# Performance work log

Measured on AMD Instinct MI355X. Metric: run time of the kernel, lower is better.

## Reference

```python
import jax, jax.numpy as jnp
import numpy as np

NUM_EMBEDDINGS = 1024
EMBEDDING_DIM = 256
COMMITMENT_COST = 0.25
DECAY = 0.99
EPSILON = 1e-05


def setup_inputs() -> dict:
    key = jax.random.key(0)
    k1, k2, k3 = jax.random.split(key, 3)
    z = jax.random.normal(k1, (32, EMBEDDING_DIM, 32, 32), dtype=jnp.float32)
    codebook = jax.random.normal(k2, (NUM_EMBEDDINGS, EMBEDDING_DIM), dtype=jnp.float32)
    ema_cluster_size = jnp.zeros((NUM_EMBEDDINGS,), dtype=jnp.float32)
    ema_dw = jax.random.normal(k3, (NUM_EMBEDDINGS, EMBEDDING_DIM), dtype=jnp.float32)
    return {"z": z, "codebook": codebook, "ema_cluster_size": ema_cluster_size, "ema_dw": ema_dw}


def reference(z, codebook, ema_cluster_size, ema_dw):
    K, D = codebook.shape
    # (B,C,H,W) -> (B,H,W,C)
    zp = jnp.transpose(z, (0, 2, 3, 1))
    z_flat = zp.reshape(-1, D)  # [N, D]
    N = z_flat.shape[0]

    # squared L2 distances to each code: [N, K]
    distances = (jnp.sum(z_flat ** 2, axis=1, keepdims=True)
                 + jnp.sum(codebook ** 2, axis=1)
                 - 2.0 * z_flat @ codebook.T)
    idx = jnp.argmin(distances, axis=1)  # [N]

    quantized = codebook[idx].reshape(zp.shape)  # [B,H,W,C]

    # training-mode EMA codebook update (one-hot scatter expressed as segment sums)
    counts = jax.ops.segment_sum(jnp.ones((N,), z_flat.dtype), idx, num_segments=K)  # encodings.sum(0)
    dw = jax.ops.segment_sum(z_flat, idx, num_segments=K)                            # encodings.T @ z_flat
    new_cluster_size = ema_cluster_size * DECAY + (1.0 - DECAY) * counts
    new_ema_dw = ema_dw * DECAY + (1.0 - DECAY) * dw
    n = jnp.sum(new_cluster_size)
    cluster_size = (new_cluster_size + EPSILON) / (n + K * EPSILON) * n
    new_codebook = new_ema_dw / cluster_size[:, None]

    commitment_loss = jnp.mean((zp - jax.lax.stop_gradient(quantized)) ** 2)
    loss = COMMITMENT_COST * commitment_loss

    # straight-through estimator
    quantized_st = zp + jax.lax.stop_gradient(quantized - zp)

    avg_probs = counts / N
    perplexity = jnp.exp(-jnp.sum(avg_probs * jnp.log(avg_probs + 1e-10)))

    quantized_out = jnp.transpose(quantized_st, (0, 3, 1, 2))  # back to (B,C,H,W)
    return (quantized_out, loss, perplexity, new_codebook, new_cluster_size, new_ema_dw)
```

## Files before the change

### kernel.cpp

```cpp
#include <hip/hip_runtime.h>
#include <cfloat>
#include <cstdint>

#define B_BATCH 32
#define D_DIM   256
#define HW      1024
#define N_POS   32768
#define K_CODES 1024
#define DECAY_F   0.99f
#define ONE_M_DECAY 0.01f
#define EPS_F   1e-5f

#define OUT_Q    0
#define OUT_LOSS 8388608
#define OUT_PERP 8388609
#define OUT_CB   8388610
#define OUT_NCS  8650754
#define OUT_EDW  8651778


#define WS_COUNTS  0
#define WS_ZNORM   4096
#define WS_BSUM    4100
#define WS_MEMSET  4104
#define WS_CBNORM  4352
#define WS_OFFS    8448
#define WS_CURSOR  12544
#define WS_IDX     16640
#define WS_SORTED  147712
#define WS_CBHI    278784
#define WS_CBLO    803072
#define WS_PART    1327360
#define WS_SCODE   3424512
#define WS_TOTAL   3555584

typedef short s16x8 __attribute__((ext_vector_type(8)));
typedef float f32x4 __attribute__((ext_vector_type(4)));
typedef unsigned long long u64;

__device__ __forceinline__ ushort f2bf_rne(float x) {
    uint u = __float_as_uint(x);
    uint r = (u + 0x7FFF + ((u >> 16) & 1)) >> 16;
    return (ushort)r;
}
__device__ __forceinline__ float bf2f(ushort h) {
    return __uint_as_float(((uint)h) << 16);
}

__device__ __forceinline__ void gload16(const void* g, void* l) {
    __builtin_amdgcn_global_load_lds(
        (const __attribute__((address_space(1))) unsigned*)(uintptr_t)g,
        (__attribute__((address_space(3))) unsigned*)(uintptr_t)l, 16, 0, 0);
}

__global__ __launch_bounds__(256) void prep_ztrans(const float* __restrict__ z,
                                                   const float* __restrict__ cb,
                                                   ushort* __restrict__ zhi,
                                                   ushort* __restrict__ zlo,
                                                   ushort* __restrict__ cbhi,
                                                   ushort* __restrict__ cblo,
                                                   float* __restrict__ cbnorm,
                                                   float* __restrict__ znorm_acc) {
    __shared__ float Zs[2][32][68];
    __shared__ float red[256];
    const int tid = threadIdx.x;

    if (blockIdx.x >= 512) {
        int wave = tid >> 6;
        int lane = tid & 63;
        int k = (blockIdx.x - 512) * 4 + wave;
        float4 v = *(const float4*)&cb[(size_t)k * D_DIM + lane * 4];
        ushort4 h, l;
        h.x = f2bf_rne(v.x); l.x = f2bf_rne(v.x - bf2f(h.x));
        h.y = f2bf_rne(v.y); l.y = f2bf_rne(v.y - bf2f(h.y));
        h.z = f2bf_rne(v.z); l.z = f2bf_rne(v.z - bf2f(h.z));
        h.w = f2bf_rne(v.w); l.w = f2bf_rne(v.w - bf2f(h.w));
        *(ushort4*)&cbhi[(size_t)k * D_DIM + lane * 4] = h;
        *(ushort4*)&cblo[(size_t)k * D_DIM + lane * 4] = l;
        float s = v.x * v.x + v.y * v.y + v.z * v.z + v.w * v.w;
        #pragma unroll
        for (int off = 32; off >= 1; off >>= 1) s += __shfl_xor(s, off);
        if (lane == 0) cbnorm[k] = s;
        return;
    }

    const int n0  = blockIdx.x * 64;
    const int b   = n0 >> 10;
    const int hw0 = n0 & 1023;
    const float* zb = z + (size_t)b * (D_DIM * HW) + hw0;

    const int zd  = tid >> 4;
    const int zcg = tid & 15;
    const int ga  = zcg ^ (((zd >> 3) & 3) << 1);
    const int gb  = zcg ^ ((((zd + 16) >> 3) & 3) << 1);
    const int n   = tid >> 2;
    const int dq  = tid & 3;
    const int zcol = (((n >> 2) ^ (dq << 1)) << 2) | (n & 3);
    float zsum = 0.f;

    {
        float4 va = *(const float4*)&zb[(size_t)zd * HW + zcg * 4];
        float4 vb = *(const float4*)&zb[(size_t)(zd + 16) * HW + zcg * 4];
        *(float4*)&Zs[0][zd][ga * 4] = va;
        *(float4*)&Zs[0][zd + 16][gb * 4] = vb;
    }

    for (int it = 0; it < 8; ++it) {
        const int d0 = it * 32;
        __syncthreads();
        float4 na, nb;
        if (it < 7) {
            na = *(const float4*)&zb[(size_t)(d0 + 32 + zd) * HW + zcg * 4];
            nb = *(const float4*)&zb[(size_t)(d0 + 48 + zd) * HW + zcg * 4];
        }
        {
            s16x8 hv, lv;
            #pragma unroll
            for (int j = 0; j < 8; ++j) {
                float f = Zs[it & 1][dq * 8 + j][zcol];
                zsum += f * f;
                ushort hb = f2bf_rne(f);
                ushort lb = f2bf_rne(f - bf2f(hb));
                hv[j] = (short)hb;
                lv[j] = (short)lb;
            }
            *(s16x8*)&zhi[(size_t)(n0 + n) * D_DIM + d0 + dq * 8] = hv;
            *(s16x8*)&zlo[(size_t)(n0 + n) * D_DIM + d0 + dq * 8] = lv;
        }
        if (it < 7) {
            *(float4*)&Zs[(it + 1) & 1][zd][ga * 4] = na;
            *(float4*)&Zs[(it + 1) & 1][zd + 16][gb * 4] = nb;
        }
    }
    red[tid] = zsum;
    __syncthreads();
    for (int s2 = 128; s2 >= 1; s2 >>= 1) {
        if (tid < s2) red[tid] += red[tid + s2];
        __syncthreads();
    }
    if (tid == 0) atomicAdd(znorm_acc, red[0]);
}

__global__ __launch_bounds__(512, 2) void argmin_gemm(const ushort* __restrict__ cbhi,
                                                      const ushort* __restrict__ cblo,
                                                      const ushort* __restrict__ zhi,
                                                      const ushort* __restrict__ zlo,
                                                      const float* __restrict__ cbnorm,
                                                      u64* __restrict__ partial) {
    __shared__ __align__(16) ushort lds[65536];

    const int tid  = threadIdx.x;
    const int wave = tid >> 6;
    const int lane = tid & 63;
    const int col  = lane & 15;
    const int lg   = lane >> 4;
    const int wr   = wave >> 2;
    const int wc   = wave & 3;
    const int blk  = blockIdx.x;
    const int mt = (blk >> 3) & 3;
    const int pt = (blk & 7) | ((blk >> 5) << 3);

    const int srow = tid >> 2;
    const int G    = tid & 3;
    const int sg   = (G ^ ((srow >> 1) & 3)) * 16;
    const char* pAh = (const char*)cbhi + (size_t)(mt * 256 + srow) * 512 + sg;
    const char* pAl = (const char*)cblo + (size_t)(mt * 256 + srow) * 512 + sg;
    const char* pBh = (const char*)zhi  + (size_t)(pt * 256 + srow) * 512 + sg;
    const char* pBl = (const char*)zlo  + (size_t)(pt * 256 + srow) * 512 + sg;
    char* const ldsw = (char*)lds + wave * 1024;

    auto stage_q = [&](int kt, int bsel, int q) {
        char* d = ldsw + bsel * 65536;
        const int kb = kt * 64;
        if (q == 0)      { gload16(pAh + kb, d);         gload16(pAh + kb + 65536, d + 8192);  }
        else if (q == 1) { gload16(pAl + kb, d + 16384); gload16(pAl + kb + 65536, d + 24576); }
        else if (q == 2) { gload16(pBh + kb, d + 32768); gload16(pBh + kb + 65536, d + 40960); }
        else             { gload16(pBl + kb, d + 49152); gload16(pBl + kb + 65536, d + 57344); }
    };

    const char* ldsc = (const char*)lds;
    const int swz  = (lg ^ ((col >> 1) & 3)) * 16;
    const int aoff = (wr * 128 + col) * 64 + swz;
    const int boff = (wc * 64 + col) * 64 + swz;

    f32x4 acc[8][4];
    #pragma unroll
    for (int mi = 0; mi < 8; ++mi)
        #pragma unroll
        for (int ni = 0; ni < 4; ++ni) acc[mi][ni] = {0.f, 0.f, 0.f, 0.f};

    stage_q(0, 0, 0); stage_q(0, 0, 1); stage_q(0, 0, 2); stage_q(0, 0, 3);

#define MM3A(AH, AL, mi, ni)                                                                   \
    acc[mi][ni] = __builtin_amdgcn_mfma_f32_16x16x32_bf16(AH, bh[ni], acc[mi][ni], 0, 0, 0);   \
    acc[mi][ni] = __builtin_amdgcn_mfma_f32_16x16x32_bf16(AH, bl[ni], acc[mi][ni], 0, 0, 0);   \
    acc[mi][ni] = __builtin_amdgcn_mfma_f32_16x16x32_bf16(AL, bh[ni], acc[mi][ni], 0, 0, 0);
#define ROW3(AH, AL, mi) MM3A(AH, AL, mi, 0) MM3A(AH, AL, mi, 1) MM3A(AH, AL, mi, 2) MM3A(AH, AL, mi, 3)

    #pragma unroll
    for (int t = 0; t < 8; ++t) {
        asm volatile("s_waitcnt vmcnt(0)" ::: "memory");
        __builtin_amdgcn_s_barrier();
        __builtin_amdgcn_sched_barrier(0);

        const char* bp = ldsc + (t & 1) * 65536;
        const int nb = (t + 1) & 1;
        s16x8 bh[4], bl[4];
        s16x8 ah0, al0, ah1, al1;

        bh[0] = *(const s16x8*)(bp + 32768 + boff);
        bl[0] = *(const s16x8*)(bp + 49152 + boff);
        bh[1] = *(const s16x8*)(bp + 32768 + boff + 1024);
        bl[1] = *(const s16x8*)(bp + 49152 + boff + 1024);
        bh[2] = *(const s16x8*)(bp + 32768 + boff + 2048);
        bl[2] = *(const s16x8*)(bp + 49152 + boff + 2048);
        bh[3] = *(const s16x8*)(bp + 32768 + boff + 3072);
        bl[3] = *(const s16x8*)(bp + 49152 + boff + 3072);
        ah0 = *(const s16x8*)(bp + aoff);
        al0 = *(const s16x8*)(bp + 16384 + aoff);
        ah1 = *(const s16x8*)(bp + aoff + 1024);
        al1 = *(const s16x8*)(bp + 16384 + aoff + 1024);
        if (t < 7) stage_q(t + 1, nb, 0);
        __builtin_amdgcn_s_setprio(1);
        ROW3(ah0, al0, 0) ROW3(ah1, al1, 1)
        __builtin_amdgcn_s_setprio(0);

        ah0 = *(const s16x8*)(bp + aoff + 2048);
        al0 = *(const s16x8*)(bp + 16384 + aoff + 2048);
        ah1 = *(const s16x8*)(bp + aoff + 3072);
        al1 = *(const s16x8*)(bp + 16384 + aoff + 3072);
        if (t < 7) stage_q(t + 1, nb, 1);
        __builtin_amdgcn_s_setprio(1);
        ROW3(ah0, al0, 2) ROW3(ah1, al1, 3)
        __builtin_amdgcn_s_setprio(0);

        ah0 = *(const s16x8*)(bp + aoff + 4096);
        al0 = *(const s16x8*)(bp + 16384 + aoff + 4096);
        ah1 = *(const s16x8*)(bp + aoff + 5120);
        al1 = *(const s16x8*)(bp + 16384 + aoff + 5120);
        if (t < 7) stage_q(t + 1, nb, 2);
        __builtin_amdgcn_s_setprio(1);
        ROW3(ah0, al0, 4) ROW3(ah1, al1, 5)
        __builtin_amdgcn_s_setprio(0);

        ah0 = *(const s16x8*)(bp + aoff + 6144);
        al0 = *(const s16x8*)(bp + 16384 + aoff + 6144);
        ah1 = *(const s16x8*)(bp + aoff + 7168);
        al1 = *(const s16x8*)(bp + 16384 + aoff + 7168);
        if (t < 7) stage_q(t + 1, nb, 3);
        __builtin_amdgcn_s_setprio(1);
        ROW3(ah0, al0, 6) ROW3(ah1, al1, 7)
        __builtin_amdgcn_s_setprio(0);
    }
#undef ROW3
#undef MM3A

    const int kbase = mt * 256 + wr * 128;
    u64 best[4] = {~0ull, ~0ull, ~0ull, ~0ull};
    #pragma unroll
    for (int mi = 0; mi < 8; ++mi) {
        float4 cn = *(const float4*)&cbnorm[kbase + mi * 16 + lg * 4];
        const float* cnp = (const float*)&cn;
        #pragma unroll
        for (int ni = 0; ni < 4; ++ni) {
            #pragma unroll
            for (int r = 0; r < 4; ++r) {
                float dist = cnp[r] - 2.f * acc[mi][ni][r];
                uint ub = __float_as_uint(dist);
                ub = ub ^ (uint)(((int)ub >> 31) | 0x80000000);
                u64 key = ((u64)ub << 32) | (uint)(kbase + mi * 16 + lg * 4 + r);
                if (key < best[ni]) best[ni] = key;
            }
        }
    }
    #pragma unroll
    for (int ni = 0; ni < 4; ++ni) {
        u64 o = __shfl_xor(best[ni], 16); if (o < best[ni]) best[ni] = o;
        o = __shfl_xor(best[ni], 32); if (o < best[ni]) best[ni] = o;
    }
    u64* kredp = (u64*)lds;
    if (lane < 16) {
        #pragma unroll
        for (int ni = 0; ni < 4; ++ni)
            kredp[(wc * 64 + ni * 16 + lane) * 2 + wr] = best[ni];
    }
    __syncthreads();
    if (tid < 256) {
        u64 a = kredp[tid * 2 + 0];
        u64 b = kredp[tid * 2 + 1]; if (b < a) a = b;
        partial[(size_t)(pt * 256 + tid) * 4 + mt] = a;
    }
}

__global__ __launch_bounds__(256) void combine_kernel(const u64* __restrict__ partial,
                                                      int* __restrict__ idx,
                                                      float* __restrict__ counts,
                                                      float* __restrict__ bsum_acc) {
    __shared__ int hist[1024];
    __shared__ float red[256];
    const int tid = threadIdx.x;
    for (int j = tid; j < 1024; j += 256) hist[j] = 0;
    __syncthreads();
    int n = blockIdx.x * 256 + tid;
    const u64* p = partial + (size_t)n * 4;
    u64 m = p[0];
    #pragma unroll
    for (int j = 1; j < 4; ++j) { u64 v = p[j]; if (v < m) m = v; }
    int k = (int)(m & 1023u);
    idx[n] = k;
    atomicAdd(&hist[k], 1);
    uint ub = (uint)(m >> 32);
    uint u = (ub & 0x80000000u) ? (ub ^ 0x80000000u) : ~ub;
    red[tid] = __uint_as_float(u);
    __syncthreads();
    for (int s2 = 128; s2 >= 1; s2 >>= 1) {
        if (tid < s2) red[tid] += red[tid + s2];
        __syncthreads();
    }
    if (tid == 0) atomicAdd(bsum_acc, red[0]);
    for (int j = tid; j < 1024; j += 256) {
        int c = hist[j];
        if (c) atomicAdd(&counts[j], (float)c);
    }
}

__global__ __launch_bounds__(1024) void small_kernel(const float* __restrict__ ema_cs,
                                                     const float* __restrict__ counts,
                                                     const float* __restrict__ znorm,
                                                     const float* __restrict__ bsum,
                                                     float* __restrict__ out_ncs,
                                                     float* __restrict__ out_perp,
                                                     float* __restrict__ out_loss,
                                                     float* __restrict__ ntot_ws,
                                                     int* __restrict__ offsets,
                                                     int* __restrict__ cursor) {
    __shared__ float s1[1024];
    __shared__ float s2[1024];
    __shared__ int   s3[1024];
    int k = threadIdx.x;
    float cnt = counts[k];
    float ncs = ema_cs[k] * DECAY_F + ONE_M_DECAY * cnt;
    out_ncs[k] = ncs;
    float p = cnt / (float)N_POS;
    s1[k] = ncs;
    s2[k] = p * logf(p + 1e-10f);
    int c = (int)cnt;
    s3[k] = c;
    __syncthreads();
    for (int off = 1; off < 1024; off <<= 1) {
        int v = (k >= off) ? s3[k - off] : 0;
        __syncthreads();
        s3[k] += v;
        __syncthreads();
    }
    int excl = s3[k] - c;
    offsets[k] = excl;
    cursor[k] = excl;
    for (int st = 512; st >= 1; st >>= 1) {
        if (k < st) { s1[k] += s1[k + st]; s2[k] += s2[k + st]; }
        __syncthreads();
    }
    if (k == 0) {
        ntot_ws[0] = s1[0];
        out_perp[0] = expf(-s2[0]);
        out_loss[0] = 0.25f * (znorm[0] + bsum[0]) / 8388608.0f;
    }
}

__global__ __launch_bounds__(256) void scatter_kernel(const int* __restrict__ idx,
                                                      int* __restrict__ cursor,
                                                      int* __restrict__ sorted,
                                                      int* __restrict__ scode,
                                                      float* __restrict__ dw_zero) {
    __shared__ int hist[1024];
    __shared__ int base_s[1024];
    const int tid = threadIdx.x;
    {
        float4 z4 = {0.f, 0.f, 0.f, 0.f};
        size_t e = ((size_t)blockIdx.x * 256 + tid) * 8;
        *(float4*)&dw_zero[e] = z4;
        *(float4*)&dw_zero[e + 4] = z4;
    }
    for (int j = tid; j < 1024; j += 256) hist[j] = 0;
    __syncthreads();
    int n = blockIdx.x * 256 + tid;
    int k = idx[n];
    atomicAdd(&hist[k], 1);
    __syncthreads();
    for (int j = tid; j < 1024; j += 256) {
        int c = hist[j];
        if (c) base_s[j] = atomicAdd(&cursor[j], c);
        hist[j] = 0;
    }
    __syncthreads();
    int rank = atomicAdd(&hist[k], 1);
    int pos = base_s[k] + rank;
    sorted[pos] = n;
    scode[pos] = k;
}

#define DW_CHUNK 64
__global__ __launch_bounds__(256) void dw_chunk_kernel(const ushort* __restrict__ zhi,
                                                       const ushort* __restrict__ zlo,
                                                       const int* __restrict__ sorted,
                                                       const int* __restrict__ scode,
                                                       const int* __restrict__ offsets,
                                                       const float* __restrict__ counts,
                                                       float* __restrict__ dw) {
    __shared__ int sid[DW_CHUNK];
    __shared__ int sk[DW_CHUNK];
    const int tid = threadIdx.x;
    const int p0 = blockIdx.x * DW_CHUNK;
    if (tid < DW_CHUNK) {
        sid[tid] = sorted[p0 + tid];
        sk[tid]  = scode[p0 + tid];
    }
    __syncthreads();
    float acc = 0.f;
    int runstart = 0;
    #pragma unroll 4
    for (int i = 0; i < DW_CHUNK; ++i) {
        int id = sid[i];
        float zv = bf2f(zhi[(size_t)id * D_DIM + tid]) + bf2f(zlo[(size_t)id * D_DIM + tid]);
        acc += zv;
        bool end = (i == DW_CHUNK - 1) || (sk[i + 1] != sk[i]);
        if (end) {
            int k = sk[i];
            int off = offsets[k];
            int cnt = (int)counts[k];
            if (p0 + runstart == off && p0 + i == off + cnt - 1)
                dw[(size_t)k * D_DIM + tid] = acc;
            else
                atomicAdd(&dw[(size_t)k * D_DIM + tid], acc);
            acc = 0.f;
            runstart = i + 1;
        }
    }
}

__global__ __launch_bounds__(256) void tail_fused(const float* __restrict__ cb,
                                                  const int* __restrict__ idx,
                                                  float* __restrict__ outq,
                                                  const float* __restrict__ ema_dw,
                                                  const float* __restrict__ out_ncs,
                                                  const float* __restrict__ ntot_ws,
                                                  float* __restrict__ out_edw,
                                                  float* __restrict__ out_cb) {
    const int tid = threadIdx.x;
    if (blockIdx.x >= 512) {
        int k = blockIdx.x - 512;
        int d = tid;
        float ncs = out_ncs[k];
        float nt = ntot_ws[0];
        float csz = (ncs + EPS_F) / (nt + (float)K_CODES * EPS_F) * nt;
        size_t e = (size_t)k * D_DIM + d;
        float ed = ema_dw[e] * DECAY_F + ONE_M_DECAY * out_edw[e];
        out_edw[e] = ed;
        out_cb[e] = ed / csz;
        return;
    }

    __shared__ float Qs[32][65];
    __shared__ int kidx[64];
    const int n0  = blockIdx.x * 64;
    const int b   = n0 >> 10;
    const int hw0 = n0 & 1023;
    float* ob = outq + (size_t)b * (D_DIM * HW) + hw0;

    if (tid < 64) kidx[tid] = idx[n0 + tid];

    for (int d0 = 0; d0 < D_DIM; d0 += 32) {
        __syncthreads();
        #pragma unroll
        for (int h = 0; h < 2; ++h) {
            int s  = tid + 256 * h;
            int n  = s >> 3;
            int dq = s & 7;
            int k  = kidx[n];
            float4 q = *(const float4*)&cb[(size_t)k * D_DIM + d0 + dq * 4];
            Qs[dq * 4 + 0][n] = q.x;
            Qs[dq * 4 + 1][n] = q.y;
            Qs[dq * 4 + 2][n] = q.z;
            Qs[dq * 4 + 3][n] = q.w;
        }
        __syncthreads();
        #pragma unroll
        for (int j = 0; j < 8; ++j) {
            int v = tid + 256 * j;
            int d = v >> 6;
            int n = v & 63;
            ob[(size_t)(d0 + d) * HW + n] = Qs[d][n];
        }
    }
}

extern "C" void kernel_launch(void* const* d_in, const int* in_sizes, int n_in,
                              void* d_out, int out_size, void* d_ws, size_t ws_size,
                              hipStream_t stream) {
    const float* z       = (const float*)d_in[0];
    const float* cb      = (const float*)d_in[1];
    const float* ema_cs  = (const float*)d_in[2];
    const float* ema_dw  = (const float*)d_in[3];
    float* out = (float*)d_out;

    char* ws = (char*)d_ws;
    float* ws_counts = (float*)(ws + WS_COUNTS);
    float* ws_znorm  = (float*)(ws + WS_ZNORM);
    float* ws_bsum   = (float*)(ws + WS_BSUM);
    float* ws_cbnorm = (float*)(ws + WS_CBNORM);
    int*   ws_offs   = (int*)(ws + WS_OFFS);
    int*   ws_cursor = (int*)(ws + WS_CURSOR);
    int*   ws_idx    = (int*)(ws + WS_IDX);
    int*   ws_sorted = (int*)(ws + WS_SORTED);
    ushort* ws_cbhi  = (ushort*)(ws + WS_CBHI);
    ushort* ws_cblo  = (ushort*)(ws + WS_CBLO);
    u64*   ws_part   = (u64*)(ws + WS_PART);
    int*   ws_scode  = (int*)(ws + WS_SCODE);

    ushort* zhi = (ushort*)out;
    ushort* zlo = zhi + 8388608;

    hipMemsetAsync(d_ws, 0, WS_MEMSET, stream);

    prep_ztrans<<<768, 256, 0, stream>>>(z, cb, zhi, zlo, ws_cbhi, ws_cblo,
                                         ws_cbnorm, ws_znorm);
    argmin_gemm<<<512, 512, 0, stream>>>(ws_cbhi, ws_cblo, zhi, zlo, ws_cbnorm, ws_part);
    combine_kernel<<<N_POS / 256, 256, 0, stream>>>(ws_part, ws_idx, ws_counts, ws_bsum);
    small_kernel<<<1, 1024, 0, stream>>>(ema_cs, ws_counts, ws_znorm, ws_bsum,
                                         out + OUT_NCS, out + OUT_PERP, out + OUT_LOSS,
                                         (float*)(ws + WS_ZNORM) + 1024, ws_offs, ws_cursor);
    scatter_kernel<<<N_POS / 256, 256, 0, stream>>>(ws_idx, ws_cursor, ws_sorted,
                                                    ws_scode, out + OUT_EDW);
    dw_chunk_kernel<<<N_POS / DW_CHUNK, 256, 0, stream>>>(zhi, zlo, ws_sorted, ws_scode,
                                                          ws_offs, ws_counts, out + OUT_EDW);
    tail_fused<<<1536, 256, 0, stream>>>(cb, ws_idx, out + OUT_Q, ema_dw, out + OUT_NCS,
                                         (float*)(ws + WS_ZNORM) + 1024,
                                         out + OUT_EDW, out + OUT_CB);
}
```

Measured before the change: 200.0 us.

## Fuse combine and small kernels via last-block ticket, drop memset and atomics

Replaces the float atomics on the norm, bsum and count accumulators with per-block partial buffers. A done-counter ticket lets the last combine block do the work of the old single-block small kernel: it sums the histograms, computes the EMA cluster sizes, perplexity, loss and the prefix-sum offsets. This removes the memset and one kernel launch. The cost is a serial 128-way histogram reduction inside one block, and the code relies on threadfence ordering for correctness.

```diff
diff --git a/kernel.cpp b/kernel.cpp
--- a/kernel.cpp
+++ b/kernel.cpp
@@ -20,9 +20,6 @@
 
 
 #define WS_COUNTS  0
-#define WS_ZNORM   4096
-#define WS_BSUM    4100
-#define WS_MEMSET  4104
 #define WS_CBNORM  4352
 #define WS_OFFS    8448
 #define WS_CURSOR  12544
@@ -31,6 +28,11 @@
 #define WS_CBHI    278784
 #define WS_CBLO    803072
 #define WS_PART    1327360
+#define WS_HIST    2375936
+#define WS_ZPART   2900224
+#define WS_BPART   2902272
+#define WS_DONE    2902784
+#define WS_NTOT    2902788
 #define WS_SCODE   3424512
 #define WS_TOTAL   3555584
 
@@ -60,10 +62,13 @@
                                                    ushort* __restrict__ cbhi,
                                                    ushort* __restrict__ cblo,
                                                    float* __restrict__ cbnorm,
-                                                   float* __restrict__ znorm_acc) {
+                                                   float* __restrict__ znorm_parts,
+                                                   int* __restrict__ done_ctr) {
     __shared__ float Zs[2][32][68];
     __shared__ float red[256];
     const int tid = threadIdx.x;
+
+    if (blockIdx.x == 0 && tid == 0) *done_ctr = 0;
 
     if (blockIdx.x >= 512) {
         int wave = tid >> 6;
@@ -138,7 +143,7 @@
         if (tid < s2) red[tid] += red[tid + s2];
         __syncthreads();
     }
-    if (tid == 0) atomicAdd(znorm_acc, red[0]);
+    if (tid == 0) znorm_parts[blockIdx.x] = red[0];
 }
 
 __global__ __launch_bounds__(512, 2) void argmin_gemm(const ushort* __restrict__ cbhi,
@@ -292,16 +297,31 @@
     }
 }
 
-__global__ __launch_bounds__(256) void combine_kernel(const u64* __restrict__ partial,
-                                                      int* __restrict__ idx,
-                                                      float* __restrict__ counts,
-                                                      float* __restrict__ bsum_acc) {
+__global__ __launch_bounds__(256) void combine2(const u64* __restrict__ partial,
+                                                int* __restrict__ idx,
+                                                const float* __restrict__ ema_cs,
+                                                const float* __restrict__ znorm_parts,
+                                                float* __restrict__ bsum_parts,
+                                                int* __restrict__ hist_ws,
+                                                int* __restrict__ done_ctr,
+                                                float* __restrict__ counts,
+                                                float* __restrict__ out_ncs,
+                                                float* __restrict__ out_perp,
+                                                float* __restrict__ out_loss,
+                                                float* __restrict__ ntot_ws,
+                                                int* __restrict__ offsets,
+                                                int* __restrict__ cursor) {
     __shared__ int hist[1024];
     __shared__ float red[256];
+    __shared__ float red2[256];
+    __shared__ int sc[256];
+    __shared__ int ticket_s;
     const int tid = threadIdx.x;
+    const int blk = blockIdx.x;
+
     for (int j = tid; j < 1024; j += 256) hist[j] = 0;
     __syncthreads();
-    int n = blockIdx.x * 256 + tid;
+    int n = blk * 256 + tid;
     const u64* p = partial + (size_t)n * 4;
     u64 m = p[0];
     #pragma unroll
@@ -317,53 +337,67 @@
         if (tid < s2) red[tid] += red[tid + s2];
         __syncthreads();
     }
-    if (tid == 0) atomicAdd(bsum_acc, red[0]);
-    for (int j = tid; j < 1024; j += 256) {
-        int c = hist[j];
-        if (c) atomicAdd(&counts[j], (float)c);
-    }
-}
-
-__global__ __launch_bounds__(1024) void small_kernel(const float* __restrict__ ema_cs,
-                                                     const float* __restrict__ counts,
-                                                     const float* __restrict__ znorm,
-                                                     const float* __restrict__ bsum,
-                                                     float* __restrict__ out_ncs,
-                                                     float* __restrict__ out_perp,
-                                                     float* __restrict__ out_loss,
-                                                     float* __restrict__ ntot_ws,
-                                                     int* __restrict__ offsets,
-                                                     int* __restrict__ cursor) {
-    __shared__ float s1[1024];
-    __shared__ float s2[1024];
-    __shared__ int   s3[1024];
-    int k = threadIdx.x;
-    float cnt = counts[k];
-    float ncs = ema_cs[k] * DECAY_F + ONE_M_DECAY * cnt;
-    out_ncs[k] = ncs;
-    float p = cnt / (float)N_POS;
-    s1[k] = ncs;
-    s2[k] = p * logf(p + 1e-10f);
-    int c = (int)cnt;
-    s3[k] = c;
-    __syncthreads();
-    for (int off = 1; off < 1024; off <<= 1) {
-        int v = (k >= off) ? s3[k - off] : 0;
-        __syncthreads();
-        s3[k] += v;
-        __syncthreads();
-    }
-    int excl = s3[k] - c;
-    offsets[k] = excl;
-    cursor[k] = excl;
-    for (int st = 512; st >= 1; st >>= 1) {
-        if (k < st) { s1[k] += s1[k + st]; s2[k] += s2[k + st]; }
-        __syncthreads();
-    }
-    if (k == 0) {
-        ntot_ws[0] = s1[0];
-        out_perp[0] = expf(-s2[0]);
-        out_loss[0] = 0.25f * (znorm[0] + bsum[0]) / 8388608.0f;
+    if (tid == 0) bsum_parts[blk] = red[0];
+    for (int j = tid; j < 1024; j += 256) hist_ws[blk * 1024 + j] = hist[j];
+
+    __threadfence();
+    __syncthreads();
+    if (tid == 0) ticket_s = atomicAdd(done_ctr, 1);
+    __syncthreads();
+    if (ticket_s != 127) return;
+    __threadfence();
+
+    float s1 = 0.f, s2 = 0.f;
+    int loc[4];
+    int tot = 0;
+    #pragma unroll
+    for (int j = 0; j < 4; ++j) {
+        int k4 = tid * 4 + j;
+        int c = 0;
+        for (int b2 = 0; b2 < 128; ++b2) c += hist_ws[b2 * 1024 + k4];
+        counts[k4] = (float)c;
+        float ncs = ema_cs[k4] * DECAY_F + ONE_M_DECAY * (float)c;
+        out_ncs[k4] = ncs;
+        s1 += ncs;
+        float pp = (float)c / (float)N_POS;
+        s2 += pp * logf(pp + 1e-10f);
+        loc[j] = tot;
+        tot += c;
+    }
+    sc[tid] = tot;
+    __syncthreads();
+    for (int off = 1; off < 256; off <<= 1) {
+        int v = (tid >= off) ? sc[tid - off] : 0;
+        __syncthreads();
+        sc[tid] += v;
+        __syncthreads();
+    }
+    int excl = sc[tid] - tot;
+    #pragma unroll
+    for (int j = 0; j < 4; ++j) {
+        offsets[tid * 4 + j] = excl + loc[j];
+        cursor[tid * 4 + j]  = excl + loc[j];
+    }
+    red[tid]  = s1;
+    red2[tid] = s2;
+    __syncthreads();
+    for (int st = 128; st >= 1; st >>= 1) {
+        if (tid < st) { red[tid] += red[tid + st]; red2[tid] += red2[tid + st]; }
+        __syncthreads();
+    }
+    float S1 = red[0], S2 = red2[0];
+    __syncthreads();
+    red[tid]  = znorm_parts[tid] + znorm_parts[tid + 256];
+    red2[tid] = (tid < 128) ? bsum_parts[tid] : 0.f;
+    __syncthreads();
+    for (int st = 128; st >= 1; st >>= 1) {
+        if (tid < st) { red[tid] += red[tid + st]; red2[tid] += red2[tid + st]; }
+        __syncthreads();
+    }
+    if (tid == 0) {
+        ntot_ws[0] = S1;
+        out_perp[0] = expf(-S2);
+        out_loss[0] = 0.25f * (red[0] + red2[0]) / 8388608.0f;
     }
 }
 
@@ -505,8 +539,6 @@
 
     char* ws = (char*)d_ws;
     float* ws_counts = (float*)(ws + WS_COUNTS);
-    float* ws_znorm  = (float*)(ws + WS_ZNORM);
-    float* ws_bsum   = (float*)(ws + WS_BSUM);
     float* ws_cbnorm = (float*)(ws + WS_CBNORM);
     int*   ws_offs   = (int*)(ws + WS_OFFS);
     int*   ws_cursor = (int*)(ws + WS_CURSOR);
@@ -515,25 +547,28 @@
     ushort* ws_cbhi  = (ushort*)(ws + WS_CBHI);
     ushort* ws_cblo  = (ushort*)(ws + WS_CBLO);
     u64*   ws_part   = (u64*)(ws + WS_PART);
+    int*   ws_hist   = (int*)(ws + WS_HIST);
+    float* ws_zpart  = (float*)(ws + WS_ZPART);
+    float* ws_bpart  = (float*)(ws + WS_BPART);
+    int*   ws_done   = (int*)(ws + WS_DONE);
+    float* ws_ntot   = (float*)(ws + WS_NTOT);
     int*   ws_scode  = (int*)(ws + WS_SCODE);
 
     ushort* zhi = (ushort*)out;
     ushort* zlo = zhi + 8388608;
 
-    hipMemsetAsync(d_ws, 0, WS_MEMSET, stream);
-
     prep_ztrans<<<768, 256, 0, stream>>>(z, cb, zhi, zlo, ws_cbhi, ws_cblo,
-                                         ws_cbnorm, ws_znorm);
+                                         ws_cbnorm, ws_zpart, ws_done);
     argmin_gemm<<<512, 512, 0, stream>>>(ws_cbhi, ws_cblo, zhi, zlo, ws_cbnorm, ws_part);
-    combine_kernel<<<N_POS / 256, 256, 0, stream>>>(ws_part, ws_idx, ws_counts, ws_bsum);
-    small_kernel<<<1, 1024, 0, stream>>>(ema_cs, ws_counts, ws_znorm, ws_bsum,
-                                         out + OUT_NCS, out + OUT_PERP, out + OUT_LOSS,
-                                         (float*)(ws + WS_ZNORM) + 1024, ws_offs, ws_cursor);
+    combine2<<<128, 256, 0, stream>>>(ws_part, ws_idx, ema_cs, ws_zpart, ws_bpart,
+                                      ws_hist, ws_done, ws_counts,
+                                      out + OUT_NCS, out + OUT_PERP, out + OUT_LOSS,
+                                      ws_ntot, ws_offs, ws_cursor);
     scatter_kernel<<<N_POS / 256, 256, 0, stream>>>(ws_idx, ws_cursor, ws_sorted,
                                                     ws_scode, out + OUT_EDW);
     dw_chunk_kernel<<<N_POS / DW_CHUNK, 256, 0, stream>>>(zhi, zlo, ws_sorted, ws_scode,
                                                           ws_offs, ws_counts, out + OUT_EDW);
-    tail_fused<<<1536, 256, 0, stream>>>(cb, ws_idx, out + OUT_Q, ema_dw, out + OUT_NCS,
-                                         (float*)(ws + WS_ZNORM) + 1024,
+    tail_fused<<<1536, 256, 0, stream>>>(cb, ws_idx, out + OUT_Q, ema_dw,
+                                         out + OUT_NCS, ws_ntot,
                                          out + OUT_EDW, out + OUT_CB);
 }
```

After: 224.5 us. +12.3%, slower.
